# Optimization experiments

Measured on AMD Instinct MI355X. Metric: run time of the kernel, lower is better.

The kernel has to match this reference:

```python
import jax, jax.numpy as jnp
import numpy as np

THRESHOLD = 0.59275


def setup_inputs() -> dict:
    key = jax.random.key(0)
    k4, k8, k16 = jax.random.split(key, 3)
    # [n_color_distances=3, batch=64, num_patches, box, box]
    x4 = jax.random.uniform(k4, (3, 64, 4096, 4, 4), dtype=jnp.float32)
    x8 = jax.random.uniform(k8, (3, 64, 1024, 8, 8), dtype=jnp.float32)
    x16 = jax.random.uniform(k16, (3, 64, 256, 16, 16), dtype=jnp.float32)
    return {"x4": x4, "x8": x8, "x16": x16}


def _percolation_q(x):
    # x: [C, B, P, b, b] -> per-patch occupancy fraction -> threshold -> mean over patches
    b = x.shape[-1]
    frac = jnp.sum(x, axis=(-2, -1)) / float(b * b)          # [C, B, P]
    q = (frac >= THRESHOLD).astype(jnp.float32)               # [C, B, P]
    return jnp.mean(q, axis=-1)                               # [C, B]


def reference(x4, x8, x16):
    # Output mirrors list[color][box] of [batch] vectors: one [n_color, batch]
    # array per box size.
    return (_percolation_q(x4), _percolation_q(x8), _percolation_q(x16))
```

## Files before the change

### kernel.cpp

```cpp
#include <hip/hip_runtime.h>


#define PERC_THRESHOLD 0.59275f

template <int B>
__device__ __forceinline__ void perc_body(const float* __restrict__ x,
                                          float* __restrict__ out,
                                          float invP) {
    constexpr int LPP = (B * B) / 4;
    constexpr int ITERS = 8;
    const int tid = threadIdx.x;
    const int lane = tid & 63;
    const float4* __restrict__ xv = (const float4*)x;
    const long long base = (long long)blockIdx.x * (256 * ITERS);
    const float thr = PERC_THRESHOLD * (float)(B * B);

    int cnt = 0;
#pragma unroll
    for (int j = 0; j < ITERS; ++j) {
        float4 v = xv[base + (long long)j * 256 + tid];
        float s = (v.x + v.y) + (v.z + v.w);
#pragma unroll
        for (int off = 1; off < LPP; off <<= 1)
            s += __shfl_xor(s, off, 64);
        if ((lane & (LPP - 1)) == 0 && s >= thr) cnt++;
    }

#pragma unroll
    for (int off = 32; off > 0; off >>= 1)
        cnt += __shfl_down(cnt, off, 64);

    __shared__ int wsum[4];
    if (lane == 0) wsum[tid >> 6] = cnt;
    __syncthreads();
    if (tid == 0) {
        float total = (float)(wsum[0] + wsum[1] + wsum[2] + wsum[3]);
        atomicAdd(&out[blockIdx.x >> 3], total * invP);
    }
}

__global__ __launch_bounds__(256)
void PercolationQ_31885837205970_kernel(const float* __restrict__ x4,
                                        const float* __restrict__ x8,
                                        const float* __restrict__ x16,
                                        float* __restrict__ out) {
    if (blockIdx.y == 0)      perc_body<4>(x4,  out,        1.0f / 4096.0f);
    else if (blockIdx.y == 1) perc_body<8>(x8,  out + 192,  1.0f / 1024.0f);
    else                      perc_body<16>(x16, out + 384, 1.0f / 256.0f);
}

extern "C" void kernel_launch(void* const* d_in, const int* in_sizes, int n_in,
                              void* d_out, int out_size, void* d_ws, size_t ws_size,
                              hipStream_t stream) {
    const float* x4  = (const float*)d_in[0];
    const float* x8  = (const float*)d_in[1];
    const float* x16 = (const float*)d_in[2];
    float* out = (float*)d_out;

    hipMemsetAsync(d_out, 0, (size_t)out_size * sizeof(float), stream);

    dim3 grid(1536, 3), block(256);
    hipLaunchKernelGGL(PercolationQ_31885837205970_kernel, grid, block, 0, stream,
                       x4, x8, x16, out);
}
```

Measured before the change: 158.8 us.

## Assign one thread per patch and count threshold hits with wave ballot

Replaces the lane-group shuffle reduction, where several lanes cooperatively summed a patch, with one thread summing a whole patch through sequential float4 loads into four accumulators. Per-wave counts now come from a ballot plus popcount. All three box sizes are flattened into one 1D grid, with block ranges mapped to each tensor. This removes the shuffle trees, but lanes now read addresses strided by the patch size, which can hurt coalescing for the 8x8 and 16x16 inputs. Work per thread also becomes uneven across the three tensors.

Result: no change. 161.2 us (+1.5%).

```diff
diff --git a/kernel.cpp b/kernel.cpp
--- a/kernel.cpp
+++ b/kernel.cpp
@@ -3,40 +3,21 @@
 
 #define PERC_THRESHOLD 0.59275f
 
-template <int B>
-__device__ __forceinline__ void perc_body(const float* __restrict__ x,
-                                          float* __restrict__ out,
-                                          float invP) {
-    constexpr int LPP = (B * B) / 4;
-    constexpr int ITERS = 8;
-    const int tid = threadIdx.x;
-    const int lane = tid & 63;
-    const float4* __restrict__ xv = (const float4*)x;
-    const long long base = (long long)blockIdx.x * (256 * ITERS);
-    const float thr = PERC_THRESHOLD * (float)(B * B);
-
-    int cnt = 0;
+template <int NV>
+__device__ __forceinline__ float patch_sum(const float4* __restrict__ xv, int base) {
+    float s0 = 0.f, s1 = 0.f, s2 = 0.f, s3 = 0.f;
 #pragma unroll
-    for (int j = 0; j < ITERS; ++j) {
-        float4 v = xv[base + (long long)j * 256 + tid];
-        float s = (v.x + v.y) + (v.z + v.w);
-#pragma unroll
-        for (int off = 1; off < LPP; off <<= 1)
-            s += __shfl_xor(s, off, 64);
-        if ((lane & (LPP - 1)) == 0 && s >= thr) cnt++;
+    for (int k = 0; k < NV; k += 4) {
+        float4 a = xv[base + k + 0];
+        float4 b = xv[base + k + 1];
+        float4 c = xv[base + k + 2];
+        float4 d = xv[base + k + 3];
+        s0 += (a.x + a.y) + (a.z + a.w);
+        s1 += (b.x + b.y) + (b.z + b.w);
+        s2 += (c.x + c.y) + (c.z + c.w);
+        s3 += (d.x + d.y) + (d.z + d.w);
     }
-
-#pragma unroll
-    for (int off = 32; off > 0; off >>= 1)
-        cnt += __shfl_down(cnt, off, 64);
-
-    __shared__ int wsum[4];
-    if (lane == 0) wsum[tid >> 6] = cnt;
-    __syncthreads();
-    if (tid == 0) {
-        float total = (float)(wsum[0] + wsum[1] + wsum[2] + wsum[3]);
-        atomicAdd(&out[blockIdx.x >> 3], total * invP);
-    }
+    return (s0 + s1) + (s2 + s3);
 }
 
 __global__ __launch_bounds__(256)
@@ -44,9 +25,46 @@
                                         const float* __restrict__ x8,
                                         const float* __restrict__ x16,
                                         float* __restrict__ out) {
-    if (blockIdx.y == 0)      perc_body<4>(x4,  out,        1.0f / 4096.0f);
-    else if (blockIdx.y == 1) perc_body<8>(x8,  out + 192,  1.0f / 1024.0f);
-    else                      perc_body<16>(x16, out + 384, 1.0f / 256.0f);
+    const int bx = blockIdx.x;
+    const int tid = threadIdx.x;
+
+    bool pred;
+    int row;
+    float invP;
+    float* o;
+
+    if (bx < 192) {
+        const float4* xv = (const float4*)x16;
+        int base = (bx * 256 + tid) * 64;
+        float s = patch_sum<64>(xv, base);
+        pred = s * (1.0f / 256.0f) >= PERC_THRESHOLD;
+        row = bx; invP = 1.0f / 256.0f; o = out + 384;
+    } else if (bx < 960) {
+        const float4* xv = (const float4*)x8;
+        int b = bx - 192;
+        int base = (b * 256 + tid) * 16;
+        float s = patch_sum<16>(xv, base);
+        pred = s * (1.0f / 64.0f) >= PERC_THRESHOLD;
+        row = b >> 2; invP = 1.0f / 1024.0f; o = out + 192;
+    } else {
+        const float4* xv = (const float4*)x4;
+        int b = bx - 960;
+        int base = (b * 256 + tid) * 4;
+        float s = patch_sum<4>(xv, base);
+        pred = s * (1.0f / 16.0f) >= PERC_THRESHOLD;
+        row = b >> 4; invP = 1.0f / 4096.0f; o = out;
+    }
+
+    unsigned long long m = __ballot(pred);
+    int cnt = __popcll(m);
+
+    __shared__ int wsum[4];
+    if ((tid & 63) == 0) wsum[tid >> 6] = cnt;
+    __syncthreads();
+    if (tid == 0) {
+        float total = (float)(wsum[0] + wsum[1] + wsum[2] + wsum[3]);
+        atomicAdd(&o[row], total * invP);
+    }
 }
 
 extern "C" void kernel_launch(void* const* d_in, const int* in_sizes, int n_in,
@@ -59,7 +77,7 @@
 
     hipMemsetAsync(d_out, 0, (size_t)out_size * sizeof(float), stream);
 
-    dim3 grid(1536, 3), block(256);
+    dim3 grid(4032), block(256);
     hipLaunchKernelGGL(PercolationQ_31885837205970_kernel, grid, block, 0, stream,
                        x4, x8, x16, out);
 }
```

## Assign one block per output row, drop memset and atomics, batch loads

Applied to the files above, without the earlier changes.

Replaces the 1536x3 grid of small 256-thread blocks with 576 blocks of 512 threads. Each block reduces one whole (color,batch) row of 256 KB and writes its result directly, so the memset launch and the atomicAdds go away. Eight float4 loads are issued together per thread before any reduction to raise memory-level parallelism, and ballot/popcount replaces the per-lane counter. The risk is that 576 large blocks give coarser load balance across CUs and fewer blocks in flight than before.

New measurement: 162.8 us. 2.5% more time.

```diff
diff --git a/kernel.cpp b/kernel.cpp
--- a/kernel.cpp
+++ b/kernel.cpp
@@ -3,50 +3,89 @@
 
 #define PERC_THRESHOLD 0.59275f
 
-template <int B>
-__device__ __forceinline__ void perc_body(const float* __restrict__ x,
-                                          float* __restrict__ out,
-                                          float invP) {
-    constexpr int LPP = (B * B) / 4;
-    constexpr int ITERS = 8;
-    const int tid = threadIdx.x;
-    const int lane = tid & 63;
-    const float4* __restrict__ xv = (const float4*)x;
-    const long long base = (long long)blockIdx.x * (256 * ITERS);
-    const float thr = PERC_THRESHOLD * (float)(B * B);
-
-    int cnt = 0;
-#pragma unroll
-    for (int j = 0; j < ITERS; ++j) {
-        float4 v = xv[base + (long long)j * 256 + tid];
-        float s = (v.x + v.y) + (v.z + v.w);
-#pragma unroll
-        for (int off = 1; off < LPP; off <<= 1)
-            s += __shfl_xor(s, off, 64);
-        if ((lane & (LPP - 1)) == 0 && s >= thr) cnt++;
-    }
-
-#pragma unroll
-    for (int off = 32; off > 0; off >>= 1)
-        cnt += __shfl_down(cnt, off, 64);
-
-    __shared__ int wsum[4];
-    if (lane == 0) wsum[tid >> 6] = cnt;
-    __syncthreads();
-    if (tid == 0) {
-        float total = (float)(wsum[0] + wsum[1] + wsum[2] + wsum[3]);
-        atomicAdd(&out[blockIdx.x >> 3], total * invP);
-    }
-}
-
-__global__ __launch_bounds__(256)
+__global__ __launch_bounds__(512)
 void PercolationQ_31885837205970_kernel(const float* __restrict__ x4,
                                         const float* __restrict__ x8,
                                         const float* __restrict__ x16,
                                         float* __restrict__ out) {
-    if (blockIdx.y == 0)      perc_body<4>(x4,  out,        1.0f / 4096.0f);
-    else if (blockIdx.y == 1) perc_body<8>(x8,  out + 192,  1.0f / 1024.0f);
-    else                      perc_body<16>(x16, out + 384, 1.0f / 256.0f);
+    const int r = blockIdx.x;
+    const int t = threadIdx.x;
+    const int lane = t & 63;
+
+    const float4* __restrict__ src;
+    int type;
+    float invB2;
+    float* o;
+    float invP;
+
+    if (r < 192) {
+        src = (const float4*)x16 + (size_t)r * 16384;
+        type = 2; invB2 = 1.0f / 256.0f; o = out + 384 + r; invP = 1.0f / 256.0f;
+    } else if (r < 384) {
+        int b = r - 192;
+        src = (const float4*)x8 + (size_t)b * 16384;
+        type = 1; invB2 = 1.0f / 64.0f; o = out + 192 + b; invP = 1.0f / 1024.0f;
+    } else {
+        int b = r - 384;
+        src = (const float4*)x4 + (size_t)b * 16384;
+        type = 0; invB2 = 1.0f / 16.0f; o = out + b; invP = 1.0f / 4096.0f;
+    }
+
+    int cnt = 0;
+#pragma unroll
+    for (int base = 0; base < 32; base += 8) {
+        float4 v[8];
+#pragma unroll
+        for (int k = 0; k < 8; ++k)
+            v[k] = src[(size_t)(base + k) * 512 + t];
+
+        float s[8];
+#pragma unroll
+        for (int k = 0; k < 8; ++k)
+            s[k] = (v[k].x + v[k].y) + (v[k].z + v[k].w);
+
+        if (type == 0) {
+#pragma unroll
+            for (int k = 0; k < 8; ++k) {
+                float a = s[k] + __shfl_xor(s[k], 1, 64);
+                a += __shfl_xor(a, 2, 64);
+                bool p = ((lane & 3) == 0) && (a * invB2 >= PERC_THRESHOLD);
+                cnt += __popcll(__ballot(p));
+            }
+        } else if (type == 1) {
+#pragma unroll
+            for (int k = 0; k < 8; ++k) {
+                float a = s[k] + __shfl_xor(s[k], 1, 64);
+                a += __shfl_xor(a, 2, 64);
+                a += __shfl_xor(a, 4, 64);
+                a += __shfl_xor(a, 8, 64);
+                bool p = ((lane & 15) == 0) && (a * invB2 >= PERC_THRESHOLD);
+                cnt += __popcll(__ballot(p));
+            }
+        } else {
+#pragma unroll
+            for (int k = 0; k < 8; ++k) {
+                float a = s[k] + __shfl_xor(s[k], 1, 64);
+                a += __shfl_xor(a, 2, 64);
+                a += __shfl_xor(a, 4, 64);
+                a += __shfl_xor(a, 8, 64);
+                a += __shfl_xor(a, 16, 64);
+                a += __shfl_xor(a, 32, 64);
+                bool p = (lane == 0) && (a * invB2 >= PERC_THRESHOLD);
+                cnt += __popcll(__ballot(p));
+            }
+        }
+    }
+
+    __shared__ int wsum[8];
+    if (lane == 0) wsum[t >> 6] = cnt;
+    __syncthreads();
+    if (t == 0) {
+        int total = 0;
+#pragma unroll
+        for (int w = 0; w < 8; ++w) total += wsum[w];
+        *o = (float)total * invP;
+    }
 }
 
 extern "C" void kernel_launch(void* const* d_in, const int* in_sizes, int n_in,
@@ -57,9 +96,7 @@
     const float* x16 = (const float*)d_in[2];
     float* out = (float*)d_out;
 
-    hipMemsetAsync(d_out, 0, (size_t)out_size * sizeof(float), stream);
-
-    dim3 grid(1536, 3), block(256);
+    dim3 grid(576), block(512);
     hipLaunchKernelGGL(PercolationQ_31885837205970_kernel, grid, block, 0, stream,
                        x4, x8, x16, out);
 }
```

## Load 256 contiguous bytes per thread with inline asm, reduce patches in-register

Applied to the files above, without the earlier changes.

Each thread now reads 64 contiguous floats through sixteen inline-asm dwordx4 loads issued back to back before a single wait, so more memory traffic is in flight per thread. Patch sums are mostly reduced within one thread instead of through cross-lane shuffles, with a few shuffles kept for 16x16 patches. The grid becomes 1D with twice the work per block, ordered largest box first. The cost is higher register use and fewer blocks, which may reduce occupancy.

Result: slower. 167.2 us (+5.3%).

```diff
diff --git a/kernel.cpp b/kernel.cpp
--- a/kernel.cpp
+++ b/kernel.cpp
@@ -1,29 +1,103 @@
 #include <hip/hip_runtime.h>
+#include <stdint.h>
 
 
 #define PERC_THRESHOLD 0.59275f
 
-template <int B>
-__device__ __forceinline__ void perc_body(const float* __restrict__ x,
-                                          float* __restrict__ out,
-                                          float invP) {
-    constexpr int LPP = (B * B) / 4;
-    constexpr int ITERS = 8;
+typedef float f4v __attribute__((ext_vector_type(4)));
+
+__global__ __launch_bounds__(256)
+void PercolationQ_31885837205970_kernel(const float* __restrict__ x4,
+                                        const float* __restrict__ x8,
+                                        const float* __restrict__ x16,
+                                        float* __restrict__ out) {
+    const int bx = blockIdx.x;
     const int tid = threadIdx.x;
     const int lane = tid & 63;
-    const float4* __restrict__ xv = (const float4*)x;
-    const long long base = (long long)blockIdx.x * (256 * ITERS);
-    const float thr = PERC_THRESHOLD * (float)(B * B);
+
+    const float* base;
+    int type, row;
+    float* o;
+    float invP;
+
+    if (bx < 768) {
+        base = x16;  type = 2;  row = bx >> 2;
+        o = out + 384; invP = 1.0f / 256.0f;
+        base += ((size_t)bx << 14);
+    } else if (bx < 1536) {
+        int b = bx - 768;
+        base = x8;   type = 1;  row = b >> 2;
+        o = out + 192; invP = 1.0f / 1024.0f;
+        base += ((size_t)b << 14);
+    } else {
+        int b = bx - 1536;
+        base = x4;   type = 0;  row = b >> 2;
+        o = out;       invP = 1.0f / 4096.0f;
+        base += ((size_t)b << 14);
+    }
+
+    uint64_t addr = (uint64_t)(base + (tid << 6));
+
+    f4v v0, v1, v2, v3, v4, v5, v6, v7, v8, v9, v10, v11, v12, v13, v14, v15;
+    asm volatile("global_load_dwordx4 %0, %1, off            " : "=v"(v0)  : "v"(addr));
+    asm volatile("global_load_dwordx4 %0, %1, off offset:16  " : "=v"(v1)  : "v"(addr));
+    asm volatile("global_load_dwordx4 %0, %1, off offset:32  " : "=v"(v2)  : "v"(addr));
+    asm volatile("global_load_dwordx4 %0, %1, off offset:48  " : "=v"(v3)  : "v"(addr));
+    asm volatile("global_load_dwordx4 %0, %1, off offset:64  " : "=v"(v4)  : "v"(addr));
+    asm volatile("global_load_dwordx4 %0, %1, off offset:80  " : "=v"(v5)  : "v"(addr));
+    asm volatile("global_load_dwordx4 %0, %1, off offset:96  " : "=v"(v6)  : "v"(addr));
+    asm volatile("global_load_dwordx4 %0, %1, off offset:112 " : "=v"(v7)  : "v"(addr));
+    asm volatile("global_load_dwordx4 %0, %1, off offset:128 " : "=v"(v8)  : "v"(addr));
+    asm volatile("global_load_dwordx4 %0, %1, off offset:144 " : "=v"(v9)  : "v"(addr));
+    asm volatile("global_load_dwordx4 %0, %1, off offset:160 " : "=v"(v10) : "v"(addr));
+    asm volatile("global_load_dwordx4 %0, %1, off offset:176 " : "=v"(v11) : "v"(addr));
+    asm volatile("global_load_dwordx4 %0, %1, off offset:192 " : "=v"(v12) : "v"(addr));
+    asm volatile("global_load_dwordx4 %0, %1, off offset:208 " : "=v"(v13) : "v"(addr));
+    asm volatile("global_load_dwordx4 %0, %1, off offset:224 " : "=v"(v14) : "v"(addr));
+    asm volatile("global_load_dwordx4 %0, %1, off offset:240 " : "=v"(v15) : "v"(addr));
+    asm volatile("s_waitcnt vmcnt(0)"
+                 : "+v"(v0), "+v"(v1), "+v"(v2), "+v"(v3),
+                   "+v"(v4), "+v"(v5), "+v"(v6), "+v"(v7),
+                   "+v"(v8), "+v"(v9), "+v"(v10), "+v"(v11),
+                   "+v"(v12), "+v"(v13), "+v"(v14), "+v"(v15));
+
+    const float s0  = (v0.x + v0.y) + (v0.z + v0.w);
+    const float s1  = (v1.x + v1.y) + (v1.z + v1.w);
+    const float s2  = (v2.x + v2.y) + (v2.z + v2.w);
+    const float s3  = (v3.x + v3.y) + (v3.z + v3.w);
+    const float s4  = (v4.x + v4.y) + (v4.z + v4.w);
+    const float s5  = (v5.x + v5.y) + (v5.z + v5.w);
+    const float s6  = (v6.x + v6.y) + (v6.z + v6.w);
+    const float s7  = (v7.x + v7.y) + (v7.z + v7.w);
+    const float s8  = (v8.x + v8.y) + (v8.z + v8.w);
+    const float s9  = (v9.x + v9.y) + (v9.z + v9.w);
+    const float s10 = (v10.x + v10.y) + (v10.z + v10.w);
+    const float s11 = (v11.x + v11.y) + (v11.z + v11.w);
+    const float s12 = (v12.x + v12.y) + (v12.z + v12.w);
+    const float s13 = (v13.x + v13.y) + (v13.z + v13.w);
+    const float s14 = (v14.x + v14.y) + (v14.z + v14.w);
+    const float s15 = (v15.x + v15.y) + (v15.z + v15.w);
 
     int cnt = 0;
-#pragma unroll
-    for (int j = 0; j < ITERS; ++j) {
-        float4 v = xv[base + (long long)j * 256 + tid];
-        float s = (v.x + v.y) + (v.z + v.w);
-#pragma unroll
-        for (int off = 1; off < LPP; off <<= 1)
-            s += __shfl_xor(s, off, 64);
-        if ((lane & (LPP - 1)) == 0 && s >= thr) cnt++;
+    if (type == 0) {
+        float p0 = (s0 + s1) + (s2 + s3);
+        float p1 = (s4 + s5) + (s6 + s7);
+        float p2 = (s8 + s9) + (s10 + s11);
+        float p3 = (s12 + s13) + (s14 + s15);
+        cnt = (p0 * (1.0f / 16.0f) >= PERC_THRESHOLD)
+            + (p1 * (1.0f / 16.0f) >= PERC_THRESHOLD)
+            + (p2 * (1.0f / 16.0f) >= PERC_THRESHOLD)
+            + (p3 * (1.0f / 16.0f) >= PERC_THRESHOLD);
+    } else {
+        float t = (((s0 + s1) + (s2 + s3)) + ((s4 + s5) + (s6 + s7)))
+                + (((s8 + s9) + (s10 + s11)) + ((s12 + s13) + (s14 + s15)));
+        if (type == 1) {
+            cnt = (t * (1.0f / 64.0f) >= PERC_THRESHOLD);
+        } else {
+            float a = t + __shfl_xor(t, 1, 64);
+            a += __shfl_xor(a, 2, 64);
+            cnt = ((lane & 3) == 0) && (a * (1.0f / 256.0f) >= PERC_THRESHOLD);
+        }
     }
 
 #pragma unroll
@@ -35,18 +109,8 @@
     __syncthreads();
     if (tid == 0) {
         float total = (float)(wsum[0] + wsum[1] + wsum[2] + wsum[3]);
-        atomicAdd(&out[blockIdx.x >> 3], total * invP);
+        atomicAdd(&o[row], total * invP);
     }
-}
-
-__global__ __launch_bounds__(256)
-void PercolationQ_31885837205970_kernel(const float* __restrict__ x4,
-                                        const float* __restrict__ x8,
-                                        const float* __restrict__ x16,
-                                        float* __restrict__ out) {
-    if (blockIdx.y == 0)      perc_body<4>(x4,  out,        1.0f / 4096.0f);
-    else if (blockIdx.y == 1) perc_body<8>(x8,  out + 192,  1.0f / 1024.0f);
-    else                      perc_body<16>(x16, out + 384, 1.0f / 256.0f);
 }
 
 extern "C" void kernel_launch(void* const* d_in, const int* in_sizes, int n_in,
@@ -59,7 +123,7 @@
 
     hipMemsetAsync(d_out, 0, (size_t)out_size * sizeof(float), stream);
 
-    dim3 grid(1536, 3), block(256);
+    dim3 grid(2304), block(256);
     hipLaunchKernelGGL(PercolationQ_31885837205970_kernel, grid, block, 0, stream,
                        x4, x8, x16, out);
 }
```
